# Kernel optimization log

Hardware: AMD Instinct MI355X
Metric: run time of the kernel (lower is better)

The kernel has to match this reference:

```python
import jax, jax.numpy as jnp
import numpy as np

N_NODES = 50000
N_EDGES = 600000
H_DIM = 128
BN_EPS = 1e-5


def setup_inputs() -> dict:
    key = jax.random.key(0)
    k1, k2, k3, k4 = jax.random.split(key, 4)
    ent_emb = jax.random.normal(k1, (N_NODES, H_DIM), dtype=jnp.float32)
    # xavier_normal_ init for the 128x128 weight
    std = float(np.sqrt(2.0 / (H_DIM + H_DIM)))
    neigh_w = jax.random.normal(k2, (H_DIM, H_DIM), dtype=jnp.float32) * std
    gamma = jnp.ones((H_DIM,), dtype=jnp.float32)
    beta = jnp.zeros((H_DIM,), dtype=jnp.float32)
    src = jax.random.randint(k3, (N_EDGES,), 0, N_NODES, dtype=jnp.int32)
    dst = jax.random.randint(k4, (N_EDGES,), 0, N_NODES, dtype=jnp.int32)
    return {"ent_emb": ent_emb, "neigh_w": neigh_w, "gamma": gamma,
            "beta": beta, "src": src, "dst": dst}


def reference(ent_emb, neigh_w, gamma, beta, src, dst):
    # Edge dot-product scores: u_dot_v('emb','emb')  -> [E]
    e_src = ent_emb[src]                      # [E, H]
    e_dst = ent_emb[dst]                      # [E, H]
    scores = jnp.sum(e_src * e_dst, axis=-1)  # [E]

    # edge_softmax: softmax over incoming edges of each destination node
    seg_max = jax.ops.segment_max(scores, dst, num_segments=N_NODES)
    seg_max = jnp.where(jnp.isfinite(seg_max), seg_max, 0.0)  # nodes w/o edges
    e = jnp.exp(scores - seg_max[dst])                         # [E]
    seg_sum = jax.ops.segment_sum(e, dst, num_segments=N_NODES)
    norm = e / seg_sum[dst]                                    # [E]

    # update_all(u_mul_e, sum): weighted gather-sum aggregation
    msg = e_src * norm[:, None]                                # [E, H]
    neigh = jax.ops.segment_sum(msg, dst, num_segments=N_NODES)  # [N, H]

    # matmul + BatchNorm1d (training-mode batch stats) + tanh
    h = neigh @ neigh_w                                        # [N, H]
    mean = jnp.mean(h, axis=0)
    var = jnp.var(h, axis=0)  # biased, matches torch BN normalization
    h = (h - mean) * jax.lax.rsqrt(var + BN_EPS) * gamma + beta
    return jnp.tanh(h)
```

## Files before the change

kernel.cpp:

```cpp
#include <hip/hip_runtime.h>
#include <hip/hip_fp16.h>
#include <math.h>

#define N_NODES 50000
#define N_EDGES 600000
#define H 128
#define BN_EPS 1e-5f
#define MAXDEG 48

__global__ void k_scatter(const int* __restrict__ src, const int* __restrict__ dst,
                          int* __restrict__ cnt, int* __restrict__ slots) {
    int i = blockIdx.x * blockDim.x + threadIdx.x;
    if (i < N_EDGES) {
        int d = dst[i];
        int pos = atomicAdd(cnt + d, 1);
        if (pos < MAXDEG) slots[d * MAXDEG + pos] = src[i];
    }
}

#define F4SCALE(a, s) { (a).x *= (s); (a).y *= (s); (a).z *= (s); (a).w *= (s); }
#define F4FMA(a, e, v) { (a).x += (e)*(v).x; (a).y += (e)*(v).y; (a).z += (e)*(v).z; (a).w += (e)*(v).w; }
#define F4SHFLADD(a, msk) { (a).x += __shfl_xor((a).x, msk, 64); (a).y += __shfl_xor((a).y, msk, 64); \
                            (a).z += __shfl_xor((a).z, msk, 64); (a).w += __shfl_xor((a).w, msk, 64); }

__global__ __launch_bounds__(256) void k_fused(const float* __restrict__ emb,
                                               const int* __restrict__ cnt,
                                               const int* __restrict__ slots,
                                               float* __restrict__ neigh) {
    int wid = (blockIdx.x * blockDim.x + threadIdx.x) >> 6;
    int lane = threadIdx.x & 63;
    if (wid >= N_NODES) return;
    int g = lane >> 3;
    int l = lane & 7;

    int deg = min(cnt[wid], MAXDEG);
    int sid = slots[wid * MAXDEG + min(lane, MAXDEG - 1)];

    const float4* rd = (const float4*)(emb + (size_t)wid * H) + l * 4;
    float4 b0 = rd[0], b1 = rd[1], b2 = rd[2], b3 = rd[3];

    float m = -INFINITY, ssum = 0.0f;
    float4 acc0 = {0,0,0,0}, acc1 = {0,0,0,0}, acc2 = {0,0,0,0}, acc3 = {0,0,0,0};

    for (int cb = 0; cb < deg; cb += 8) {
        int e = cb + g;
        bool valid = e < deg;
        int s = __shfl(sid, valid ? e : 0, 64);
        const float4* rs = (const float4*)(emb + (size_t)s * H) + l * 4;
        float4 a0 = rs[0], a1 = rs[1], a2 = rs[2], a3 = rs[3];

        float v = a0.x*b0.x + a0.y*b0.y + a0.z*b0.z + a0.w*b0.w
                + a1.x*b1.x + a1.y*b1.y + a1.z*b1.z + a1.w*b1.w
                + a2.x*b2.x + a2.y*b2.y + a2.z*b2.z + a2.w*b2.w
                + a3.x*b3.x + a3.y*b3.y + a3.z*b3.z + a3.w*b3.w;
        v += __shfl_xor(v, 1, 64);
        v += __shfl_xor(v, 2, 64);
        v += __shfl_xor(v, 4, 64);
        if (!valid) v = -INFINITY;

        float cmax = v;
        cmax = fmaxf(cmax, __shfl_xor(cmax, 8, 64));
        cmax = fmaxf(cmax, __shfl_xor(cmax, 16, 64));
        cmax = fmaxf(cmax, __shfl_xor(cmax, 32, 64));
        float mnew = fmaxf(m, cmax);
        if (mnew > m) {
            float scale = __expf(m - mnew);
            ssum *= scale;
            F4SCALE(acc0, scale); F4SCALE(acc1, scale);
            F4SCALE(acc2, scale); F4SCALE(acc3, scale);
            m = mnew;
        }

        float ev = __expf(v - m);
        ssum += ev;
        F4FMA(acc0, ev, a0); F4FMA(acc1, ev, a1);
        F4FMA(acc2, ev, a2); F4FMA(acc3, ev, a3);
    }

    ssum += __shfl_xor(ssum, 8, 64);
    ssum += __shfl_xor(ssum, 16, 64);
    ssum += __shfl_xor(ssum, 32, 64);
    F4SHFLADD(acc0, 8);  F4SHFLADD(acc1, 8);  F4SHFLADD(acc2, 8);  F4SHFLADD(acc3, 8);
    F4SHFLADD(acc0, 16); F4SHFLADD(acc1, 16); F4SHFLADD(acc2, 16); F4SHFLADD(acc3, 16);
    F4SHFLADD(acc0, 32); F4SHFLADD(acc1, 32); F4SHFLADD(acc2, 32); F4SHFLADD(acc3, 32);

    float inv = (deg > 0) ? 1.0f / ssum : 0.0f;
    if (g == 0) {
        float4* po = (float4*)(neigh + (size_t)wid * H) + l * 4;
        F4SCALE(acc0, inv); F4SCALE(acc1, inv); F4SCALE(acc2, inv); F4SCALE(acc3, inv);
        po[0] = acc0; po[1] = acc1; po[2] = acc2; po[3] = acc3;
    }
}

#define MM_ROWS 128
template <bool F16>
__global__ __launch_bounds__(256, 2) void k_matmul(const float* __restrict__ neigh,
                                                   const float* __restrict__ W,
                                                   float* __restrict__ hout32,
                                                   __half* __restrict__ hout16,
                                                   float* __restrict__ stats) {
    __shared__ float Wl[H * H];
    int t = threadIdx.x;
    int n0 = blockIdx.x * MM_ROWS;
    int cg = t & 15, rg = t >> 4;
    int j0 = cg * 8;
    int r0 = n0 + rg * 8;

    for (int idx = t; idx < H * H / 4; idx += 256)
        ((float4*)Wl)[idx] = ((const float4*)W)[idx];

    const float* pr[8];
    bool valid[8];
#pragma unroll
    for (int i = 0; i < 8; ++i) {
        int n = r0 + i;
        valid[i] = (n < N_NODES);
        pr[i] = neigh + (size_t)(valid[i] ? n : 0) * H;
    }

    __syncthreads();

    float acc[8][8] = {};
    for (int k0 = 0; k0 < H; k0 += 4) {
        float4 rv[8];
#pragma unroll
        for (int i = 0; i < 8; ++i) rv[i] = *(const float4*)(pr[i] + k0);
        float4 wa[4], wb[4];
#pragma unroll
        for (int kk = 0; kk < 4; ++kk) {
            wa[kk] = *(const float4*)&Wl[(k0 + kk) * H + j0];
            wb[kk] = *(const float4*)&Wl[(k0 + kk) * H + j0 + 4];
        }
#pragma unroll
        for (int kk = 0; kk < 4; ++kk) {
#pragma unroll
            for (int i = 0; i < 8; ++i) {
                float rk = ((const float*)&rv[i])[kk];
                acc[i][0] += rk * wa[kk].x;
                acc[i][1] += rk * wa[kk].y;
                acc[i][2] += rk * wa[kk].z;
                acc[i][3] += rk * wa[kk].w;
                acc[i][4] += rk * wb[kk].x;
                acc[i][5] += rk * wb[kk].y;
                acc[i][6] += rk * wb[kk].z;
                acc[i][7] += rk * wb[kk].w;
            }
        }
    }

#pragma unroll
    for (int i = 0; i < 8; ++i) {
        if (valid[i]) {
            if (F16) {
                union { uint4 u; __half2 h2[4]; } U;
                U.h2[0] = __floats2half2_rn(acc[i][0], acc[i][1]);
                U.h2[1] = __floats2half2_rn(acc[i][2], acc[i][3]);
                U.h2[2] = __floats2half2_rn(acc[i][4], acc[i][5]);
                U.h2[3] = __floats2half2_rn(acc[i][6], acc[i][7]);
                *(uint4*)(hout16 + (size_t)(r0 + i) * H + j0) = U.u;
            } else {
                *(float4*)(hout32 + (size_t)(r0 + i) * H + j0) =
                    make_float4(acc[i][0], acc[i][1], acc[i][2], acc[i][3]);
                *(float4*)(hout32 + (size_t)(r0 + i) * H + j0 + 4) =
                    make_float4(acc[i][4], acc[i][5], acc[i][6], acc[i][7]);
            }
        }
    }

    __syncthreads();
    float* Sl = Wl;
    float* Ql = Wl + 16 * H;
#pragma unroll
    for (int c = 0; c < 8; ++c) {
        float s = 0.0f, q = 0.0f;
#pragma unroll
        for (int i = 0; i < 8; ++i) {
            if (valid[i]) { s += acc[i][c]; q += acc[i][c] * acc[i][c]; }
        }
        Sl[rg * H + j0 + c] = s;
        Ql[rg * H + j0 + c] = q;
    }
    __syncthreads();
    if (t < H) {
        float s = 0.0f;
#pragma unroll
        for (int r = 0; r < 16; ++r) s += Sl[r * H + t];
        atomicAdd(stats + t, s);
    } else {
        int j = t - H;
        float q = 0.0f;
#pragma unroll
        for (int r = 0; r < 16; ++r) q += Ql[r * H + j];
        atomicAdd(stats + 128 + j, q);
    }
}

__device__ __forceinline__ float tanh_fast(float x) {
    float e = __expf(2.0f * x);
    return 1.0f - 2.0f / (e + 1.0f);
}

__global__ __launch_bounds__(256) void k_apply_f32(float* __restrict__ h,
                                                   const float* __restrict__ stats,
                                                   const float* __restrict__ gamma,
                                                   const float* __restrict__ beta) {
    __shared__ float sc[128], sh[128];
    int t = threadIdx.x;
    if (t < 128) {
        float mean = stats[t] * (1.0f / N_NODES);
        float var = stats[128 + t] * (1.0f / N_NODES) - mean * mean;
        var = fmaxf(var, 0.0f);
        float s = gamma[t] * rsqrtf(var + BN_EPS);
        sc[t] = s;
        sh[t] = beta[t] - mean * s;
    }
    __syncthreads();
    int i = blockIdx.x * 256 + t;
    if (i < N_NODES * H / 4) {
        float4 v = ((const float4*)h)[i];
        int jb = (i & 31) * 4;
        v.x = tanh_fast(v.x * sc[jb]     + sh[jb]);
        v.y = tanh_fast(v.y * sc[jb + 1] + sh[jb + 1]);
        v.z = tanh_fast(v.z * sc[jb + 2] + sh[jb + 2]);
        v.w = tanh_fast(v.w * sc[jb + 3] + sh[jb + 3]);
        ((float4*)h)[i] = v;
    }
}

__global__ __launch_bounds__(256) void k_apply_f16(const __half* __restrict__ h,
                                                   float* __restrict__ out,
                                                   const float* __restrict__ stats,
                                                   const float* __restrict__ gamma,
                                                   const float* __restrict__ beta) {
    __shared__ float sc[128], sh[128];
    int t = threadIdx.x;
    if (t < 128) {
        float mean = stats[t] * (1.0f / N_NODES);
        float var = stats[128 + t] * (1.0f / N_NODES) - mean * mean;
        var = fmaxf(var, 0.0f);
        float s = gamma[t] * rsqrtf(var + BN_EPS);
        sc[t] = s;
        sh[t] = beta[t] - mean * s;
    }
    __syncthreads();
    int i = blockIdx.x * 256 + t;
    if (i < N_NODES * H / 8) {
        union { uint4 u; __half2 h2[4]; } U;
        U.u = ((const uint4*)h)[i];
        int jb = (i & 15) * 8;
        float2 f0 = __half22float2(U.h2[0]);
        float2 f1 = __half22float2(U.h2[1]);
        float2 f2 = __half22float2(U.h2[2]);
        float2 f3 = __half22float2(U.h2[3]);
        float4 o0, o1;
        o0.x = tanh_fast(f0.x * sc[jb]     + sh[jb]);
        o0.y = tanh_fast(f0.y * sc[jb + 1] + sh[jb + 1]);
        o0.z = tanh_fast(f1.x * sc[jb + 2] + sh[jb + 2]);
        o0.w = tanh_fast(f1.y * sc[jb + 3] + sh[jb + 3]);
        o1.x = tanh_fast(f2.x * sc[jb + 4] + sh[jb + 4]);
        o1.y = tanh_fast(f2.y * sc[jb + 5] + sh[jb + 5]);
        o1.z = tanh_fast(f3.x * sc[jb + 6] + sh[jb + 6]);
        o1.w = tanh_fast(f3.y * sc[jb + 7] + sh[jb + 7]);
        ((float4*)out)[2 * i]     = o0;
        ((float4*)out)[2 * i + 1] = o1;
    }
}

extern "C" void kernel_launch(void* const* d_in, const int* in_sizes, int n_in,
                              void* d_out, int out_size, void* d_ws, size_t ws_size,
                              hipStream_t stream) {
    const float* emb   = (const float*)d_in[0];
    const float* W     = (const float*)d_in[1];
    const float* gamma = (const float*)d_in[2];
    const float* beta  = (const float*)d_in[3];
    const int*   src   = (const int*)d_in[4];
    const int*   dst   = (const int*)d_in[5];
    float* out = (float*)d_out;

    int*    cnt   = (int*)d_ws;
    float*  stats = (float*)(cnt + N_NODES);
    int*    slots = (int*)(stats + 256) + 4;
    float*  neigh = (float*)(slots + (size_t)N_NODES * MAXDEG);
    __half* hbuf  = (__half*)(neigh + (size_t)N_NODES * H);

    size_t need_f16 = (size_t)(N_NODES + 260) * 4
                    + (size_t)N_NODES * MAXDEG * 4
                    + (size_t)N_NODES * H * 4
                    + (size_t)N_NODES * H * 2;
    bool use_f16 = ws_size >= need_f16;

    hipMemsetAsync(cnt, 0, (N_NODES + 260) * sizeof(int), stream);
    k_scatter<<<(N_EDGES + 255) / 256, 256, 0, stream>>>(src, dst, cnt, slots);
    k_fused<<<(N_NODES * 64 + 255) / 256, 256, 0, stream>>>(emb, cnt, slots, neigh);

    int nblk_mm = (N_NODES + MM_ROWS - 1) / MM_ROWS;
    if (use_f16) {
        k_matmul<true><<<nblk_mm, 256, 0, stream>>>(neigh, W, nullptr, hbuf, stats);
        k_apply_f16<<<(N_NODES * H / 8 + 255) / 256, 256, 0, stream>>>(hbuf, out, stats, gamma, beta);
    } else {
        k_matmul<false><<<nblk_mm, 256, 0, stream>>>(neigh, W, out, nullptr, stats);
        k_apply_f32<<<(N_NODES * H / 4 + 255) / 256, 256, 0, stream>>>(out, stats, gamma, beta);
    }
}
```

Measured before the change: 207.4 us.

## Gather neighbor embeddings in fp16 and store aggregated features as fp16

Converts the embedding table to fp16 inside the scatter kernel, then has the fused aggregation kernel gather source rows in fp16, halving the bytes per random row read. The aggregated neighbor features are also written in fp16 and the matmul reads them as fp16, cutting intermediate traffic. The fp32 fallback path and its workspace-size check are removed, so a larger workspace is assumed and precision drops on scores and aggregates.

```diff
diff --git a/kernel.cpp b/kernel.cpp
--- a/kernel.cpp
+++ b/kernel.cpp
@@ -9,13 +9,24 @@
 #define MAXDEG 48
 
 __global__ void k_scatter(const int* __restrict__ src, const int* __restrict__ dst,
-                          int* __restrict__ cnt, int* __restrict__ slots) {
+                          int* __restrict__ cnt, int* __restrict__ slots,
+                          const float* __restrict__ emb, __half* __restrict__ emb16) {
     int i = blockIdx.x * blockDim.x + threadIdx.x;
     if (i < N_EDGES) {
         int d = dst[i];
         int pos = atomicAdd(cnt + d, 1);
         if (pos < MAXDEG) slots[d * MAXDEG + pos] = src[i];
     }
+    if (i < N_NODES * H / 8) {
+        float4 f0 = ((const float4*)emb)[2 * i];
+        float4 f1 = ((const float4*)emb)[2 * i + 1];
+        union { uint4 u; __half2 h2[4]; } U;
+        U.h2[0] = __floats2half2_rn(f0.x, f0.y);
+        U.h2[1] = __floats2half2_rn(f0.z, f0.w);
+        U.h2[2] = __floats2half2_rn(f1.x, f1.y);
+        U.h2[3] = __floats2half2_rn(f1.z, f1.w);
+        ((uint4*)emb16)[i] = U.u;
+    }
 }
 
 #define F4SCALE(a, s) { (a).x *= (s); (a).y *= (s); (a).z *= (s); (a).w *= (s); }
@@ -24,9 +35,10 @@
                             (a).z += __shfl_xor((a).z, msk, 64); (a).w += __shfl_xor((a).w, msk, 64); }
 
 __global__ __launch_bounds__(256) void k_fused(const float* __restrict__ emb,
+                                               const __half* __restrict__ emb16,
                                                const int* __restrict__ cnt,
                                                const int* __restrict__ slots,
-                                               float* __restrict__ neigh) {
+                                               __half* __restrict__ neigh) {
     int wid = (blockIdx.x * blockDim.x + threadIdx.x) >> 6;
     int lane = threadIdx.x & 63;
     if (wid >= N_NODES) return;
@@ -46,8 +58,18 @@
         int e = cb + g;
         bool valid = e < deg;
         int s = __shfl(sid, valid ? e : 0, 64);
-        const float4* rs = (const float4*)(emb + (size_t)s * H) + l * 4;
-        float4 a0 = rs[0], a1 = rs[1], a2 = rs[2], a3 = rs[3];
+        const uint4* rs = (const uint4*)(emb16 + (size_t)s * H) + l * 2;
+        uint4 p0 = rs[0], p1 = rs[1];
+        const __half2* h0 = (const __half2*)&p0;
+        const __half2* h1 = (const __half2*)&p1;
+        float2 t0 = __half22float2(h0[0]), t1 = __half22float2(h0[1]);
+        float2 t2 = __half22float2(h0[2]), t3 = __half22float2(h0[3]);
+        float2 t4 = __half22float2(h1[0]), t5 = __half22float2(h1[1]);
+        float2 t6 = __half22float2(h1[2]), t7 = __half22float2(h1[3]);
+        float4 a0 = make_float4(t0.x, t0.y, t1.x, t1.y);
+        float4 a1 = make_float4(t2.x, t2.y, t3.x, t3.y);
+        float4 a2 = make_float4(t4.x, t4.y, t5.x, t5.y);
+        float4 a3 = make_float4(t6.x, t6.y, t7.x, t7.y);
 
         float v = a0.x*b0.x + a0.y*b0.y + a0.z*b0.z + a0.w*b0.w
                 + a1.x*b1.x + a1.y*b1.y + a1.z*b1.z + a1.w*b1.w
@@ -86,18 +108,26 @@
 
     float inv = (deg > 0) ? 1.0f / ssum : 0.0f;
     if (g == 0) {
-        float4* po = (float4*)(neigh + (size_t)wid * H) + l * 4;
         F4SCALE(acc0, inv); F4SCALE(acc1, inv); F4SCALE(acc2, inv); F4SCALE(acc3, inv);
-        po[0] = acc0; po[1] = acc1; po[2] = acc2; po[3] = acc3;
+        union { uint4 u; __half2 h2[4]; } U0, U1;
+        U0.h2[0] = __floats2half2_rn(acc0.x, acc0.y);
+        U0.h2[1] = __floats2half2_rn(acc0.z, acc0.w);
+        U0.h2[2] = __floats2half2_rn(acc1.x, acc1.y);
+        U0.h2[3] = __floats2half2_rn(acc1.z, acc1.w);
+        U1.h2[0] = __floats2half2_rn(acc2.x, acc2.y);
+        U1.h2[1] = __floats2half2_rn(acc2.z, acc2.w);
+        U1.h2[2] = __floats2half2_rn(acc3.x, acc3.y);
+        U1.h2[3] = __floats2half2_rn(acc3.z, acc3.w);
+        uint4* po = (uint4*)(neigh + (size_t)wid * H);
+        po[2 * l] = U0.u;
+        po[2 * l + 1] = U1.u;
     }
 }
 
 #define MM_ROWS 128
-template <bool F16>
-__global__ __launch_bounds__(256, 2) void k_matmul(const float* __restrict__ neigh,
+__global__ __launch_bounds__(256, 2) void k_matmul(const __half* __restrict__ neigh,
                                                    const float* __restrict__ W,
-                                                   float* __restrict__ hout32,
-                                                   __half* __restrict__ hout16,
+                                                   __half* __restrict__ hout,
                                                    float* __restrict__ stats) {
     __shared__ float Wl[H * H];
     int t = threadIdx.x;
@@ -109,7 +139,7 @@
     for (int idx = t; idx < H * H / 4; idx += 256)
         ((float4*)Wl)[idx] = ((const float4*)W)[idx];
 
-    const float* pr[8];
+    const __half* pr[8];
     bool valid[8];
 #pragma unroll
     for (int i = 0; i < 8; ++i) {
@@ -122,9 +152,17 @@
 
     float acc[8][8] = {};
     for (int k0 = 0; k0 < H; k0 += 4) {
-        float4 rv[8];
-#pragma unroll
-        for (int i = 0; i < 8; ++i) rv[i] = *(const float4*)(pr[i] + k0);
+        uint2 rv[8];
+#pragma unroll
+        for (int i = 0; i < 8; ++i) rv[i] = *(const uint2*)(pr[i] + k0);
+        float rf[8][4];
+#pragma unroll
+        for (int i = 0; i < 8; ++i) {
+            const __half2* hp = (const __half2*)&rv[i];
+            float2 x0 = __half22float2(hp[0]);
+            float2 x1 = __half22float2(hp[1]);
+            rf[i][0] = x0.x; rf[i][1] = x0.y; rf[i][2] = x1.x; rf[i][3] = x1.y;
+        }
         float4 wa[4], wb[4];
 #pragma unroll
         for (int kk = 0; kk < 4; ++kk) {
@@ -135,7 +173,7 @@
         for (int kk = 0; kk < 4; ++kk) {
 #pragma unroll
             for (int i = 0; i < 8; ++i) {
-                float rk = ((const float*)&rv[i])[kk];
+                float rk = rf[i][kk];
                 acc[i][0] += rk * wa[kk].x;
                 acc[i][1] += rk * wa[kk].y;
                 acc[i][2] += rk * wa[kk].z;
@@ -151,19 +189,12 @@
 #pragma unroll
     for (int i = 0; i < 8; ++i) {
         if (valid[i]) {
-            if (F16) {
-                union { uint4 u; __half2 h2[4]; } U;
-                U.h2[0] = __floats2half2_rn(acc[i][0], acc[i][1]);
-                U.h2[1] = __floats2half2_rn(acc[i][2], acc[i][3]);
-                U.h2[2] = __floats2half2_rn(acc[i][4], acc[i][5]);
-                U.h2[3] = __floats2half2_rn(acc[i][6], acc[i][7]);
-                *(uint4*)(hout16 + (size_t)(r0 + i) * H + j0) = U.u;
-            } else {
-                *(float4*)(hout32 + (size_t)(r0 + i) * H + j0) =
-                    make_float4(acc[i][0], acc[i][1], acc[i][2], acc[i][3]);
-                *(float4*)(hout32 + (size_t)(r0 + i) * H + j0 + 4) =
-                    make_float4(acc[i][4], acc[i][5], acc[i][6], acc[i][7]);
-            }
+            union { uint4 u; __half2 h2[4]; } U;
+            U.h2[0] = __floats2half2_rn(acc[i][0], acc[i][1]);
+            U.h2[1] = __floats2half2_rn(acc[i][2], acc[i][3]);
+            U.h2[2] = __floats2half2_rn(acc[i][4], acc[i][5]);
+            U.h2[3] = __floats2half2_rn(acc[i][6], acc[i][7]);
+            *(uint4*)(hout + (size_t)(r0 + i) * H + j0) = U.u;
         }
     }
 
@@ -198,33 +229,6 @@
 __device__ __forceinline__ float tanh_fast(float x) {
     float e = __expf(2.0f * x);
     return 1.0f - 2.0f / (e + 1.0f);
-}
-
-__global__ __launch_bounds__(256) void k_apply_f32(float* __restrict__ h,
-                                                   const float* __restrict__ stats,
-                                                   const float* __restrict__ gamma,
-                                                   const float* __restrict__ beta) {
-    __shared__ float sc[128], sh[128];
-    int t = threadIdx.x;
-    if (t < 128) {
-        float mean = stats[t] * (1.0f / N_NODES);
-        float var = stats[128 + t] * (1.0f / N_NODES) - mean * mean;
-        var = fmaxf(var, 0.0f);
-        float s = gamma[t] * rsqrtf(var + BN_EPS);
-        sc[t] = s;
-        sh[t] = beta[t] - mean * s;
-    }
-    __syncthreads();
-    int i = blockIdx.x * 256 + t;
-    if (i < N_NODES * H / 4) {
-        float4 v = ((const float4*)h)[i];
-        int jb = (i & 31) * 4;
-        v.x = tanh_fast(v.x * sc[jb]     + sh[jb]);
-        v.y = tanh_fast(v.y * sc[jb + 1] + sh[jb + 1]);
-        v.z = tanh_fast(v.z * sc[jb + 2] + sh[jb + 2]);
-        v.w = tanh_fast(v.w * sc[jb + 3] + sh[jb + 3]);
-        ((float4*)h)[i] = v;
-    }
 }
 
 __global__ __launch_bounds__(256) void k_apply_f16(const __half* __restrict__ h,
@@ -277,28 +281,18 @@
     const int*   dst   = (const int*)d_in[5];
     float* out = (float*)d_out;
 
-    int*    cnt   = (int*)d_ws;
-    float*  stats = (float*)(cnt + N_NODES);
-    int*    slots = (int*)(stats + 256) + 4;
-    float*  neigh = (float*)(slots + (size_t)N_NODES * MAXDEG);
-    __half* hbuf  = (__half*)(neigh + (size_t)N_NODES * H);
-
-    size_t need_f16 = (size_t)(N_NODES + 260) * 4
-                    + (size_t)N_NODES * MAXDEG * 4
-                    + (size_t)N_NODES * H * 4
-                    + (size_t)N_NODES * H * 2;
-    bool use_f16 = ws_size >= need_f16;
+    int*    cnt    = (int*)d_ws;
+    float*  stats  = (float*)(cnt + N_NODES);
+    int*    slots  = (int*)(stats + 256) + 4;
+    __half* neigh  = (__half*)(slots + (size_t)N_NODES * MAXDEG);
+    __half* hbuf   = neigh + (size_t)N_NODES * H;
+    __half* emb16  = hbuf + (size_t)N_NODES * H;
 
     hipMemsetAsync(cnt, 0, (N_NODES + 260) * sizeof(int), stream);
-    k_scatter<<<(N_EDGES + 255) / 256, 256, 0, stream>>>(src, dst, cnt, slots);
-    k_fused<<<(N_NODES * 64 + 255) / 256, 256, 0, stream>>>(emb, cnt, slots, neigh);
-
+    int nthr_sc = (N_NODES * H / 8 > N_EDGES) ? N_NODES * H / 8 : N_EDGES;
+    k_scatter<<<(nthr_sc + 255) / 256, 256, 0, stream>>>(src, dst, cnt, slots, emb, emb16);
+    k_fused<<<(N_NODES * 64 + 255) / 256, 256, 0, stream>>>(emb, emb16, cnt, slots, neigh);
     int nblk_mm = (N_NODES + MM_ROWS - 1) / MM_ROWS;
-    if (use_f16) {
-        k_matmul<true><<<nblk_mm, 256, 0, stream>>>(neigh, W, nullptr, hbuf, stats);
-        k_apply_f16<<<(N_NODES * H / 8 + 255) / 256, 256, 0, stream>>>(hbuf, out, stats, gamma, beta);
-    } else {
-        k_matmul<false><<<nblk_mm, 256, 0, stream>>>(neigh, W, out, nullptr, stats);
-        k_apply_f32<<<(N_NODES * H / 4 + 255) / 256, 256, 0, stream>>>(out, stats, gamma, beta);
-    }
-}
+    k_matmul<<<nblk_mm, 256, 0, stream>>>(neigh, W, hbuf, stats);
+    k_apply_f16<<<(N_NODES * H / 8 + 255) / 256, 256, 0, stream>>>(hbuf, out, stats, gamma, beta);
+}
```

Result: no change. 211.3 us (+1.9%).
